# Optimization experiments

Measured on AMD Instinct MI355X. Metric: run time of the kernel, lower is better.

The kernel has to match this reference:

```python
import jax, jax.numpy as jnp
import numpy as np

S, B, V, E, H = 512, 256, 100000, 128, 256


def setup_inputs() -> dict:
    key = jax.random.key(0)
    k1, k2, k3, k4, k5, k6 = jax.random.split(key, 6)
    X = jax.random.randint(k1, (S, B), 0, V)
    emb = jax.random.normal(k2, (V, E), dtype=jnp.float32)
    # PyTorch nn.RNN init: U(-1/sqrt(H), 1/sqrt(H))
    s = 1.0 / np.sqrt(H)
    W_ih = jax.random.uniform(k3, (H, E), minval=-s, maxval=s, dtype=jnp.float32)
    W_hh = jax.random.uniform(k4, (H, H), minval=-s, maxval=s, dtype=jnp.float32)
    b_ih = jax.random.uniform(k5, (H,), minval=-s, maxval=s, dtype=jnp.float32)
    b_hh = jax.random.uniform(k6, (H,), minval=-s, maxval=s, dtype=jnp.float32)
    return {"X": X, "emb": emb, "W_ih": W_ih, "W_hh": W_hh, "b_ih": b_ih, "b_hh": b_hh}


def reference(X, emb, W_ih, W_hh, b_ih, b_hh):
    embedded = emb[X]                                   # [S, B, E]
    # Precompute input projections for all timesteps (one big GEMM)
    xproj = jnp.einsum('sbe,he->sbh', embedded, W_ih) + b_ih + b_hh  # [S, B, H]
    h0 = jnp.zeros((B, H), dtype=embedded.dtype)

    def step(h, xp):
        h_new = jnp.tanh(xp + h @ W_hh.T)
        return h_new, None

    h_last, _ = jax.lax.scan(step, h0, xproj)           # [B, H]
    return jax.nn.log_softmax(h_last, axis=1)
```

## Files before the change

kernel.cpp:

```cpp
#include <hip/hip_runtime.h>
#include <math.h>

#define S_LEN 512
#define B_SZ  256
#define E_SZ  128
#define H_SZ  256

typedef __attribute__((ext_vector_type(8))) short bf16x8;
typedef __attribute__((ext_vector_type(4))) short bf16x4;
typedef __attribute__((ext_vector_type(4))) float f32x4;

__device__ __forceinline__ short f2bf(float f) {
    union { float f; unsigned u; } v; v.f = f;
    unsigned r = v.u + 0x7FFFu + ((v.u >> 16) & 1u);
    return (short)(r >> 16);
}

__device__ __forceinline__ float tanh_fast(float v) {
    float e = __expf(2.f * v);
    return 1.f - 2.f * __builtin_amdgcn_rcpf(e + 1.f);
}

#define K1_ROWS 64
#define K1_KP   32
#define K1_AP   (K1_ROWS + 4)
#define K1_WP   (H_SZ + 4)

__global__ __launch_bounds__(256) void embed_proj_kernel(
    const int*   __restrict__ X,
    const float* __restrict__ emb,
    const float* __restrict__ W_ih,
    const float* __restrict__ b_ih,
    const float* __restrict__ b_hh,
    float*       __restrict__ xproj)
{
    __shared__ int   toks[K1_ROWS];
    __shared__ float A_lds[K1_KP][K1_AP];
    __shared__ float W_lds[K1_KP][K1_WP];

    const int tid  = threadIdx.x;
    const int row0 = blockIdx.x * K1_ROWS;

    if (tid < K1_ROWS) toks[tid] = X[row0 + tid];

    const int r0 = (tid & 7) * 8;
    const int h0 = (tid >> 3) * 8;

    float acc[8][8];
#pragma unroll
    for (int i = 0; i < 8; ++i)
#pragma unroll
        for (int j = 0; j < 8; ++j) acc[i][j] = 0.f;

    __syncthreads();

    const int ar = tid >> 2;
    const int ak = (tid & 3) * 8;

#pragma unroll
    for (int p = 0; p < E_SZ / K1_KP; ++p) {
        {
            const float4* src = (const float4*)(emb + (size_t)toks[ar] * E_SZ + p * K1_KP + ak);
            float4 v0 = src[0], v1 = src[1];
            A_lds[ak+0][ar] = v0.x; A_lds[ak+1][ar] = v0.y;
            A_lds[ak+2][ar] = v0.z; A_lds[ak+3][ar] = v0.w;
            A_lds[ak+4][ar] = v1.x; A_lds[ak+5][ar] = v1.y;
            A_lds[ak+6][ar] = v1.z; A_lds[ak+7][ar] = v1.w;
        }
        {
            const float4* src = (const float4*)(W_ih + (size_t)tid * E_SZ + p * K1_KP);
#pragma unroll
            for (int j = 0; j < 8; ++j) {
                float4 v = src[j];
                W_lds[j*4+0][tid] = v.x; W_lds[j*4+1][tid] = v.y;
                W_lds[j*4+2][tid] = v.z; W_lds[j*4+3][tid] = v.w;
            }
        }
        __syncthreads();

#pragma unroll 4
        for (int k = 0; k < K1_KP; ++k) {
            const float4 a0 = *(const float4*)&A_lds[k][r0];
            const float4 a1 = *(const float4*)&A_lds[k][r0 + 4];
            const float4 w0 = *(const float4*)&W_lds[k][h0];
            const float4 w1 = *(const float4*)&W_lds[k][h0 + 4];
            const float av[8] = {a0.x,a0.y,a0.z,a0.w,a1.x,a1.y,a1.z,a1.w};
            const float wv[8] = {w0.x,w0.y,w0.z,w0.w,w1.x,w1.y,w1.z,w1.w};
#pragma unroll
            for (int i = 0; i < 8; ++i)
#pragma unroll
                for (int j = 0; j < 8; ++j)
                    acc[i][j] += av[i] * wv[j];
        }
        __syncthreads();
    }

    float bias[8];
#pragma unroll
    for (int j = 0; j < 8; ++j) bias[j] = b_ih[h0 + j] + b_hh[h0 + j];

#pragma unroll
    for (int i = 0; i < 8; ++i) {
        const size_t row = (size_t)(row0 + r0 + i);
        float4 o0, o1;
        o0.x = acc[i][0] + bias[0]; o0.y = acc[i][1] + bias[1];
        o0.z = acc[i][2] + bias[2]; o0.w = acc[i][3] + bias[3];
        o1.x = acc[i][4] + bias[4]; o1.y = acc[i][5] + bias[5];
        o1.z = acc[i][6] + bias[6]; o1.w = acc[i][7] + bias[7];
        *(float4*)&xproj[row * H_SZ + h0]     = o0;
        *(float4*)&xproj[row * H_SZ + h0 + 4] = o1;
    }
}

__global__ __launch_bounds__(512) void rnn_scan_kernel(
    const float* __restrict__ xproj,
    const float* __restrict__ W_hh,
    float*       __restrict__ out)
{
    const int tid  = threadIdx.x;
    const int wave = tid >> 6;
    const int lane = tid & 63;
    const int bl   = lane & 15;
    const int quad = lane >> 4;
    const int B0   = blockIdx.x * 16;

    __shared__ short HB[2][8][64][8];
    __shared__ float sred[8][16];

    bf16x8 wfrag[2][8];
#pragma unroll
    for (int mt = 0; mt < 2; ++mt) {
        const int h = wave * 32 + mt * 16 + bl;
#pragma unroll
        for (int kk = 0; kk < 8; ++kk) {
            const float* wp = W_hh + (size_t)h * H_SZ + kk * 32 + quad * 8;
            float4 x0 = *(const float4*)wp;
            float4 x1 = *(const float4*)(wp + 4);
            bf16x8 f;
            f[0] = f2bf(x0.x); f[1] = f2bf(x0.y); f[2] = f2bf(x0.z); f[3] = f2bf(x0.w);
            f[4] = f2bf(x1.x); f[5] = f2bf(x1.y); f[6] = f2bf(x1.z); f[7] = f2bf(x1.w);
            wfrag[mt][kk] = f;
        }
    }

    short* const hb0 = &HB[0][0][0][0];
    short* const hb1 = &HB[1][0][0][0];

    ((int4*)hb0)[tid] = make_int4(0, 0, 0, 0);

    const short* rd0 = hb0 + lane * 8;
    const short* rd1 = hb1 + lane * 8;

    const int wo0 = wave * 512 + (quad >> 1) * 128 + bl * 8 + (quad & 1) * 4;
    const int wo1 = wo0 + 256;
    short* w0a = hb0 + wo0; short* w0b = hb0 + wo1;
    short* w1a = hb1 + wo0; short* w1b = hb1 + wo1;

    const float* xpb = xproj + (size_t)(B0 + bl) * H_SZ + wave * 32 + quad * 4;
    f32x4 xq0 = *(const f32x4*)xpb;
    f32x4 xq1 = *(const f32x4*)(xpb + 16);
    const float* xnp = xpb + (size_t)B_SZ * H_SZ;

    __syncthreads();

    auto do_step = [&](const short* rd, short* wa, short* wb) {
        bf16x8 bf[8];
#pragma unroll
        for (int kk = 0; kk < 8; ++kk)
            bf[kk] = *(const bf16x8*)(rd + kk * 512);

        f32x4 xn0 = *(const f32x4*)xnp;
        f32x4 xn1 = *(const f32x4*)(xnp + 16);
        xnp += (size_t)B_SZ * H_SZ;

        f32x4 c0a = {0.f, 0.f, 0.f, 0.f}, c0b = {0.f, 0.f, 0.f, 0.f};
        f32x4 c1a = {0.f, 0.f, 0.f, 0.f}, c1b = {0.f, 0.f, 0.f, 0.f};
#pragma unroll
        for (int kk = 0; kk < 4; ++kk) {
            c0a = __builtin_amdgcn_mfma_f32_16x16x32_bf16(wfrag[0][kk],     bf[kk],     c0a, 0, 0, 0);
            c1a = __builtin_amdgcn_mfma_f32_16x16x32_bf16(wfrag[1][kk],     bf[kk],     c1a, 0, 0, 0);
            c0b = __builtin_amdgcn_mfma_f32_16x16x32_bf16(wfrag[0][kk + 4], bf[kk + 4], c0b, 0, 0, 0);
            c1b = __builtin_amdgcn_mfma_f32_16x16x32_bf16(wfrag[1][kk + 4], bf[kk + 4], c1b, 0, 0, 0);
        }
        const f32x4 d0 = c0a + c0b;
        const f32x4 d1 = c1a + c1b;

        float t0 = tanh_fast(d0[0] + xq0[0]);
        float t1 = tanh_fast(d0[1] + xq0[1]);
        float t2 = tanh_fast(d0[2] + xq0[2]);
        float t3 = tanh_fast(d0[3] + xq0[3]);
        float u0 = tanh_fast(d1[0] + xq1[0]);
        float u1 = tanh_fast(d1[1] + xq1[1]);
        float u2 = tanh_fast(d1[2] + xq1[2]);
        float u3 = tanh_fast(d1[3] + xq1[3]);
        unsigned p01, p23, q01, q23;
        asm("v_cvt_pk_bf16_f32 %0, %1, %2" : "=v"(p01) : "v"(t0), "v"(t1));
        asm("v_cvt_pk_bf16_f32 %0, %1, %2" : "=v"(p23) : "v"(t2), "v"(t3));
        asm("v_cvt_pk_bf16_f32 %0, %1, %2" : "=v"(q01) : "v"(u0), "v"(u1));
        asm("v_cvt_pk_bf16_f32 %0, %1, %2" : "=v"(q23) : "v"(u2), "v"(u3));
        *(uint2*)wa = make_uint2(p01, p23);
        *(uint2*)wb = make_uint2(q01, q23);

        xq0 = xn0; xq1 = xn1;
        __syncthreads();
    };

    for (int s = 0; s < 510; s += 2) {
        do_step(rd0, w1a, w1b);
        do_step(rd1, w0a, w0b);
    }
    do_step(rd0, w1a, w1b);

    float vf0[4], vf1[4];
    {
        bf16x8 bf[8];
#pragma unroll
        for (int kk = 0; kk < 8; ++kk)
            bf[kk] = *(const bf16x8*)(rd1 + kk * 512);
        f32x4 c0a = {0.f, 0.f, 0.f, 0.f}, c0b = {0.f, 0.f, 0.f, 0.f};
        f32x4 c1a = {0.f, 0.f, 0.f, 0.f}, c1b = {0.f, 0.f, 0.f, 0.f};
#pragma unroll
        for (int kk = 0; kk < 4; ++kk) {
            c0a = __builtin_amdgcn_mfma_f32_16x16x32_bf16(wfrag[0][kk],     bf[kk],     c0a, 0, 0, 0);
            c1a = __builtin_amdgcn_mfma_f32_16x16x32_bf16(wfrag[1][kk],     bf[kk],     c1a, 0, 0, 0);
            c0b = __builtin_amdgcn_mfma_f32_16x16x32_bf16(wfrag[0][kk + 4], bf[kk + 4], c0b, 0, 0, 0);
            c1b = __builtin_amdgcn_mfma_f32_16x16x32_bf16(wfrag[1][kk + 4], bf[kk + 4], c1b, 0, 0, 0);
        }
        const f32x4 d0 = c0a + c0b;
        const f32x4 d1 = c1a + c1b;
#pragma unroll
        for (int r = 0; r < 4; ++r) {
            vf0[r] = tanh_fast(d0[r] + xq0[r]);
            vf1[r] = tanh_fast(d1[r] + xq1[r]);
        }
    }

    float m = fmaxf(fmaxf(fmaxf(vf0[0], vf0[1]), fmaxf(vf0[2], vf0[3])),
                    fmaxf(fmaxf(vf1[0], vf1[1]), fmaxf(vf1[2], vf1[3])));
    m = fmaxf(m, __shfl_xor(m, 16));
    m = fmaxf(m, __shfl_xor(m, 32));
    if (lane < 16) sred[wave][bl] = m;
    __syncthreads();
    float mall = sred[0][bl];
#pragma unroll
    for (int w = 1; w < 8; ++w) mall = fmaxf(mall, sred[w][bl]);
    __syncthreads();

    float ss = 0.f;
#pragma unroll
    for (int r = 0; r < 4; ++r)
        ss += __expf(vf0[r] - mall) + __expf(vf1[r] - mall);
    ss += __shfl_xor(ss, 16);
    ss += __shfl_xor(ss, 32);
    if (lane < 16) sred[wave][bl] = ss;
    __syncthreads();
    float tot = sred[0][bl];
#pragma unroll
    for (int w = 1; w < 8; ++w) tot += sred[w][bl];
    const float lse = mall + __logf(tot);

    f32x4 o0, o1;
#pragma unroll
    for (int r = 0; r < 4; ++r) { o0[r] = vf0[r] - lse; o1[r] = vf1[r] - lse; }
    float* op = out + (size_t)(B0 + bl) * H_SZ + wave * 32 + quad * 4;
    *(f32x4*)op        = o0;
    *(f32x4*)(op + 16) = o1;
}

extern "C" void kernel_launch(void* const* d_in, const int* in_sizes, int n_in,
                              void* d_out, int out_size, void* d_ws, size_t ws_size,
                              hipStream_t stream) {
    const int*   X    = (const int*)  d_in[0];
    const float* emb  = (const float*)d_in[1];
    const float* W_ih = (const float*)d_in[2];
    const float* W_hh = (const float*)d_in[3];
    const float* b_ih = (const float*)d_in[4];
    const float* b_hh = (const float*)d_in[5];
    float* out   = (float*)d_out;
    float* xproj = (float*)d_ws;

    embed_proj_kernel<<<dim3((S_LEN * B_SZ) / K1_ROWS), 256, 0, stream>>>(
        X, emb, W_ih, b_ih, b_hh, xproj);

    rnn_scan_kernel<<<dim3(B_SZ / 16), 512, 0, stream>>>(xproj, W_hh, out);
}
```

Baseline: 491.2 us.

## Use split-bf16 MFMA for input projection and prefetch xproj two steps ahead

The embedding projection GEMM moves from FP32 FMA on LDS tiles to bf16 MFMA. Each operand is split into high and low bf16 parts and combined with three products, which keeps close to FP32 accuracy. In the scan kernel, xproj loads are double-buffered two timesteps ahead. The step barrier becomes an explicit LDS waitcnt plus s_barrier, so global prefetch loads can stay in flight across the barrier. The costs are three times the MFMA work, extra conversion ALU in the projection, and wrap-around pointer logic that issues harmless extra loads.

```diff
diff --git a/kernel.cpp b/kernel.cpp
--- a/kernel.cpp
+++ b/kernel.cpp
@@ -15,18 +15,18 @@
     unsigned r = v.u + 0x7FFFu + ((v.u >> 16) & 1u);
     return (short)(r >> 16);
 }
+__device__ __forceinline__ float bf2f(short h) {
+    union { unsigned u; float f; } c;
+    c.u = ((unsigned)(unsigned short)h) << 16;
+    return c.f;
+}
 
 __device__ __forceinline__ float tanh_fast(float v) {
     float e = __expf(2.f * v);
     return 1.f - 2.f * __builtin_amdgcn_rcpf(e + 1.f);
 }
 
-#define K1_ROWS 64
-#define K1_KP   32
-#define K1_AP   (K1_ROWS + 4)
-#define K1_WP   (H_SZ + 4)
-
-__global__ __launch_bounds__(256) void embed_proj_kernel(
+__global__ __launch_bounds__(256, 2) void embed_proj_mfma(
     const int*   __restrict__ X,
     const float* __restrict__ emb,
     const float* __restrict__ W_ih,
@@ -34,81 +34,104 @@
     const float* __restrict__ b_hh,
     float*       __restrict__ xproj)
 {
-    __shared__ int   toks[K1_ROWS];
-    __shared__ float A_lds[K1_KP][K1_AP];
-    __shared__ float W_lds[K1_KP][K1_WP];
+    __shared__ int   toks[64];
+    __shared__ short BtH[4][4][64][8];
+    __shared__ short BtL[4][4][64][8];
 
     const int tid  = threadIdx.x;
-    const int row0 = blockIdx.x * K1_ROWS;
-
-    if (tid < K1_ROWS) toks[tid] = X[row0 + tid];
-
-    const int r0 = (tid & 7) * 8;
-    const int h0 = (tid >> 3) * 8;
-
-    float acc[8][8];
-#pragma unroll
-    for (int i = 0; i < 8; ++i)
-#pragma unroll
-        for (int j = 0; j < 8; ++j) acc[i][j] = 0.f;
-
-    __syncthreads();
-
-    const int ar = tid >> 2;
-    const int ak = (tid & 3) * 8;
-
-#pragma unroll
-    for (int p = 0; p < E_SZ / K1_KP; ++p) {
-        {
-            const float4* src = (const float4*)(emb + (size_t)toks[ar] * E_SZ + p * K1_KP + ak);
-            float4 v0 = src[0], v1 = src[1];
-            A_lds[ak+0][ar] = v0.x; A_lds[ak+1][ar] = v0.y;
-            A_lds[ak+2][ar] = v0.z; A_lds[ak+3][ar] = v0.w;
-            A_lds[ak+4][ar] = v1.x; A_lds[ak+5][ar] = v1.y;
-            A_lds[ak+6][ar] = v1.z; A_lds[ak+7][ar] = v1.w;
-        }
-        {
-            const float4* src = (const float4*)(W_ih + (size_t)tid * E_SZ + p * K1_KP);
+    const int wave = tid >> 6;
+    const int lane = tid & 63;
+    const int bl   = lane & 15;
+    const int quad = lane >> 4;
+    const size_t row0 = (size_t)blockIdx.x * 64;
+
+    if (tid < 64) toks[tid] = X[row0 + tid];
+    __syncthreads();
+
+    {
+        const int r  = tid >> 2;
+        const int kk = tid & 3;
+        const float* ep = emb + (size_t)toks[r] * E_SZ + kk * 32;
+#pragma unroll
+        for (int q = 0; q < 4; ++q) {
+            float4 a = *(const float4*)(ep + q * 8);
+            float4 b = *(const float4*)(ep + q * 8 + 4);
+            float v[8] = {a.x, a.y, a.z, a.w, b.x, b.y, b.z, b.w};
+            bf16x8 fh, fl;
 #pragma unroll
             for (int j = 0; j < 8; ++j) {
-                float4 v = src[j];
-                W_lds[j*4+0][tid] = v.x; W_lds[j*4+1][tid] = v.y;
-                W_lds[j*4+2][tid] = v.z; W_lds[j*4+3][tid] = v.w;
+                short h = f2bf(v[j]);
+                fh[j] = h;
+                fl[j] = f2bf(v[j] - bf2f(h));
             }
-        }
-        __syncthreads();
-
-#pragma unroll 4
-        for (int k = 0; k < K1_KP; ++k) {
-            const float4 a0 = *(const float4*)&A_lds[k][r0];
-            const float4 a1 = *(const float4*)&A_lds[k][r0 + 4];
-            const float4 w0 = *(const float4*)&W_lds[k][h0];
-            const float4 w1 = *(const float4*)&W_lds[k][h0 + 4];
-            const float av[8] = {a0.x,a0.y,a0.z,a0.w,a1.x,a1.y,a1.z,a1.w};
-            const float wv[8] = {w0.x,w0.y,w0.z,w0.w,w1.x,w1.y,w1.z,w1.w};
-#pragma unroll
-            for (int i = 0; i < 8; ++i)
-#pragma unroll
-                for (int j = 0; j < 8; ++j)
-                    acc[i][j] += av[i] * wv[j];
-        }
-        __syncthreads();
-    }
-
-    float bias[8];
-#pragma unroll
-    for (int j = 0; j < 8; ++j) bias[j] = b_ih[h0 + j] + b_hh[h0 + j];
-
-#pragma unroll
-    for (int i = 0; i < 8; ++i) {
-        const size_t row = (size_t)(row0 + r0 + i);
-        float4 o0, o1;
-        o0.x = acc[i][0] + bias[0]; o0.y = acc[i][1] + bias[1];
-        o0.z = acc[i][2] + bias[2]; o0.w = acc[i][3] + bias[3];
-        o1.x = acc[i][4] + bias[4]; o1.y = acc[i][5] + bias[5];
-        o1.z = acc[i][6] + bias[6]; o1.w = acc[i][7] + bias[7];
-        *(float4*)&xproj[row * H_SZ + h0]     = o0;
-        *(float4*)&xproj[row * H_SZ + h0 + 4] = o1;
+            *(bf16x8*)&BtH[r >> 4][kk][q * 16 + (r & 15)][0] = fh;
+            *(bf16x8*)&BtL[r >> 4][kk][q * 16 + (r & 15)][0] = fl;
+        }
+    }
+    __syncthreads();
+
+#pragma unroll
+    for (int mp = 0; mp < 2; ++mp) {
+        bf16x8 wh[2][4], wl[2][4];
+#pragma unroll
+        for (int i = 0; i < 2; ++i) {
+            const int h = wave * 64 + (mp * 2 + i) * 16 + bl;
+#pragma unroll
+            for (int kk = 0; kk < 4; ++kk) {
+                const float* wp = W_ih + (size_t)h * E_SZ + kk * 32 + quad * 8;
+                float4 a = *(const float4*)wp;
+                float4 b = *(const float4*)(wp + 4);
+                float v[8] = {a.x, a.y, a.z, a.w, b.x, b.y, b.z, b.w};
+                bf16x8 fh, fl;
+#pragma unroll
+                for (int j = 0; j < 8; ++j) {
+                    short hh = f2bf(v[j]);
+                    fh[j] = hh;
+                    fl[j] = f2bf(v[j] - bf2f(hh));
+                }
+                wh[i][kk] = fh; wl[i][kk] = fl;
+            }
+        }
+
+        f32x4 acc[2][4];
+#pragma unroll
+        for (int i = 0; i < 2; ++i)
+#pragma unroll
+            for (int nt = 0; nt < 4; ++nt) acc[i][nt] = (f32x4){0.f, 0.f, 0.f, 0.f};
+
+#pragma unroll
+        for (int kk = 0; kk < 4; ++kk) {
+            bf16x8 bh[4], blo[4];
+#pragma unroll
+            for (int nt = 0; nt < 4; ++nt) {
+                bh[nt]  = *(const bf16x8*)&BtH[nt][kk][lane][0];
+                blo[nt] = *(const bf16x8*)&BtL[nt][kk][lane][0];
+            }
+#pragma unroll
+            for (int i = 0; i < 2; ++i)
+#pragma unroll
+                for (int nt = 0; nt < 4; ++nt) {
+                    f32x4 a = acc[i][nt];
+                    a = __builtin_amdgcn_mfma_f32_16x16x32_bf16(wh[i][kk], bh[nt],  a, 0, 0, 0);
+                    a = __builtin_amdgcn_mfma_f32_16x16x32_bf16(wh[i][kk], blo[nt], a, 0, 0, 0);
+                    a = __builtin_amdgcn_mfma_f32_16x16x32_bf16(wl[i][kk], bh[nt],  a, 0, 0, 0);
+                    acc[i][nt] = a;
+                }
+        }
+
+#pragma unroll
+        for (int i = 0; i < 2; ++i) {
+            const int hb = wave * 64 + (mp * 2 + i) * 16 + quad * 4;
+            float4 bi = *(const float4*)&b_ih[hb];
+            float4 bh4 = *(const float4*)&b_hh[hb];
+#pragma unroll
+            for (int nt = 0; nt < 4; ++nt) {
+                f32x4 o = acc[i][nt];
+                o[0] += bi.x + bh4.x; o[1] += bi.y + bh4.y;
+                o[2] += bi.z + bh4.z; o[3] += bi.w + bh4.w;
+                *(f32x4*)&xproj[(row0 + nt * 16 + bl) * H_SZ + hb] = o;
+            }
+        }
     }
 }
 
@@ -156,22 +179,24 @@
     short* w0a = hb0 + wo0; short* w0b = hb0 + wo1;
     short* w1a = hb1 + wo0; short* w1b = hb1 + wo1;
 
+    const size_t stp = (size_t)B_SZ * H_SZ;
     const float* xpb = xproj + (size_t)(B0 + bl) * H_SZ + wave * 32 + quad * 4;
-    f32x4 xq0 = *(const f32x4*)xpb;
-    f32x4 xq1 = *(const f32x4*)(xpb + 16);
-    const float* xnp = xpb + (size_t)B_SZ * H_SZ;
-
-    __syncthreads();
-
-    auto do_step = [&](const short* rd, short* wa, short* wb) {
+
+    f32x4 xA0 = *(const f32x4*)(xpb);
+    f32x4 xA1 = *(const f32x4*)(xpb + 16);
+    f32x4 xB0 = *(const f32x4*)(xpb + stp);
+    f32x4 xB1 = *(const f32x4*)(xpb + stp + 16);
+
+    __syncthreads();
+
+    float vf0[4], vf1[4];
+
+    auto do_step = [&](const short* rd, short* wa, short* wb,
+                       f32x4& x0, f32x4& x1, const float* pf) {
         bf16x8 bf[8];
 #pragma unroll
         for (int kk = 0; kk < 8; ++kk)
             bf[kk] = *(const bf16x8*)(rd + kk * 512);
-
-        f32x4 xn0 = *(const f32x4*)xnp;
-        f32x4 xn1 = *(const f32x4*)(xnp + 16);
-        xnp += (size_t)B_SZ * H_SZ;
 
         f32x4 c0a = {0.f, 0.f, 0.f, 0.f}, c0b = {0.f, 0.f, 0.f, 0.f};
         f32x4 c1a = {0.f, 0.f, 0.f, 0.f}, c1b = {0.f, 0.f, 0.f, 0.f};
@@ -185,14 +210,14 @@
         const f32x4 d0 = c0a + c0b;
         const f32x4 d1 = c1a + c1b;
 
-        float t0 = tanh_fast(d0[0] + xq0[0]);
-        float t1 = tanh_fast(d0[1] + xq0[1]);
-        float t2 = tanh_fast(d0[2] + xq0[2]);
-        float t3 = tanh_fast(d0[3] + xq0[3]);
-        float u0 = tanh_fast(d1[0] + xq1[0]);
-        float u1 = tanh_fast(d1[1] + xq1[1]);
-        float u2 = tanh_fast(d1[2] + xq1[2]);
-        float u3 = tanh_fast(d1[3] + xq1[3]);
+        float t0 = tanh_fast(d0[0] + x0[0]);
+        float t1 = tanh_fast(d0[1] + x0[1]);
+        float t2 = tanh_fast(d0[2] + x0[2]);
+        float t3 = tanh_fast(d0[3] + x0[3]);
+        float u0 = tanh_fast(d1[0] + x1[0]);
+        float u1 = tanh_fast(d1[1] + x1[1]);
+        float u2 = tanh_fast(d1[2] + x1[2]);
+        float u3 = tanh_fast(d1[3] + x1[3]);
         unsigned p01, p23, q01, q23;
         asm("v_cvt_pk_bf16_f32 %0, %1, %2" : "=v"(p01) : "v"(t0), "v"(t1));
         asm("v_cvt_pk_bf16_f32 %0, %1, %2" : "=v"(p23) : "v"(t2), "v"(t3));
@@ -201,17 +226,25 @@
         *(uint2*)wa = make_uint2(p01, p23);
         *(uint2*)wb = make_uint2(q01, q23);
 
-        xq0 = xn0; xq1 = xn1;
-        __syncthreads();
+        x0 = *(const f32x4*)pf;
+        x1 = *(const f32x4*)(pf + 16);
+
+        asm volatile("s_waitcnt lgkmcnt(0)" ::: "memory");
+        __builtin_amdgcn_sched_barrier(0);
+        __builtin_amdgcn_s_barrier();
     };
 
+    const float* pfA = xpb + 2 * stp;
+    const float* pfB = xpb + 3 * stp;
     for (int s = 0; s < 510; s += 2) {
-        do_step(rd0, w1a, w1b);
-        do_step(rd1, w0a, w0b);
-    }
-    do_step(rd0, w1a, w1b);
-
-    float vf0[4], vf1[4];
+        do_step(rd0, w1a, w1b, xA0, xA1, pfA);
+        do_step(rd1, w0a, w0b, xB0, xB1, pfB);
+        pfA += 2 * stp; pfB += 2 * stp;
+        if (pfA > xpb + 511 * stp) pfA = xpb;
+        if (pfB > xpb + 511 * stp) pfB = xpb;
+    }
+    do_step(rd0, w1a, w1b, xA0, xA1, xpb);
+
     {
         bf16x8 bf[8];
 #pragma unroll
@@ -230,8 +263,8 @@
         const f32x4 d1 = c1a + c1b;
 #pragma unroll
         for (int r = 0; r < 4; ++r) {
-            vf0[r] = tanh_fast(d0[r] + xq0[r]);
-            vf1[r] = tanh_fast(d1[r] + xq1[r]);
+            vf0[r] = tanh_fast(d0[r] + xB0[r]);
+            vf1[r] = tanh_fast(d1[r] + xB1[r]);
         }
     }
 
@@ -279,7 +312,7 @@
     float* out   = (float*)d_out;
     float* xproj = (float*)d_ws;
 
-    embed_proj_kernel<<<dim3((S_LEN * B_SZ) / K1_ROWS), 256, 0, stream>>>(
+    embed_proj_mfma<<<dim3((S_LEN * B_SZ) / 64), 256, 0, stream>>>(
         X, emb, W_ih, b_ih, b_hh, xproj);
 
     rnn_scan_kernel<<<dim3(B_SZ / 16), 512, 0, stream>>>(xproj, W_hh, out);
```

Result: faster. 464.1 us (-5.5%).
